# Kernel tuning notes

Measured on AMD Instinct MI355X. Metric: run time of the kernel, lower is better.

Reference implementation:

```python
import jax, jax.numpy as jnp
import numpy as np

THRESHOLD = 0.5
ALPHA = 1.0
N, D = 100000, 256
B, K = 1024, 128


def _l2norm(x):
    # F.normalize(x, p=2, dim=-1) with eps=1e-12
    return x / jnp.maximum(jnp.linalg.norm(x, axis=-1, keepdims=True), 1e-12)


def setup_inputs() -> dict:
    key = jax.random.key(0)
    k1, k2, k3, k4, k5, k6, k7 = jax.random.split(key, 7)
    feature = jax.random.normal(k1, (N, D), dtype=jnp.float32)
    text_embedding = jax.random.normal(k2, (N, D), dtype=jnp.float32)
    virtual = jax.random.normal(k3, (1, D), dtype=jnp.float32)
    # Gumbel(0,1) noise for gumbel_softmax (tau=1), materialized for determinism
    u = jax.random.uniform(k4, (B, K, K), dtype=jnp.float32, minval=1e-6, maxval=1.0 - 1e-6)
    gumbel = -jnp.log(-jnp.log(u))
    ego_nodes = jnp.sort(jax.random.randint(k5, (B, K), 0, N, dtype=jnp.int32), axis=-1)
    edges_adj = jax.random.randint(k6, (B, K, K), 0, 2, dtype=jnp.int32)
    train_label = jax.random.randint(k7, (B,), 0, 2, dtype=jnp.int32)
    return {"feature": feature, "text_embedding": text_embedding, "virtual": virtual,
            "gumbel": gumbel, "ego_nodes": ego_nodes, "edges_adj": edges_adj,
            "train_label": train_label}


def reference(feature, text_embedding, virtual, gumbel, ego_nodes, edges_adj, train_label):
    feat = _l2norm(feature)          # self.feature (normalized in __init__)
    emb = _l2norm(text_embedding)    # self.embedding
    te_local = _l2norm(emb - virtual)            # [N, D]

    tb = te_local[ego_nodes]                     # [B, K, D] gather per ego-subgraph
    sim = jnp.einsum('bkd,bjd->bkj', tb, tb) - THRESHOLD   # [B, K, K]
    sim_sub = jax.nn.softmax(sim + gumbel, axis=-1)         # gumbel_softmax, tau=1

    adj = edges_adj.astype(sim_sub.dtype)        # scatter edges_adj[src,dst]=1, precomputed
    # s_diff: row-wise L2 norm then mean over rows
    s_diff = jnp.sqrt(jnp.sum((adj - sim_sub) ** 2, axis=-1)).mean(axis=-1)   # [B]

    emb_out = feat[ego_nodes].mean(axis=1)       # [B, D] sum(feature)/n
    emb_pg = emb[ego_nodes].mean(axis=1)         # [B, D] sum(embedding)/n  (n == K)
    f_diff = jnp.linalg.norm(emb_out - emb_pg, axis=-1)                        # [B]

    score = s_diff + ALPHA * f_diff
    score = (score - score.min()) / (score.max() - score.min())

    y = train_label.astype(score.dtype)
    eps = 1e-7  # stabilizes log at exact 0/1 (torch BCELoss clamps log at -100)
    sc = jnp.clip(score, eps, 1.0 - eps)
    bce = -(y * jnp.log(sc) + (1.0 - y) * jnp.log1p(-sc)).mean()
    loss = bce / y.shape[0]
    return score, loss
```

## Files before the change

kernel.cpp:

```cpp
#include <hip/hip_runtime.h>
#include <hip/hip_bf16.h>
#include <math.h>

#define DIM 256
#define BB 1024
#define KK 128
#define PITCH 264

typedef __attribute__((ext_vector_type(8))) short short8;
typedef __attribute__((ext_vector_type(4))) float float4v;

__device__ __forceinline__ float dot4(const float4 a, const float4 b) {
    return a.x*b.x + a.y*b.y + a.z*b.z + a.w*b.w;
}

__device__ __forceinline__ unsigned bf2bits(float a, float b) {
    float2 t; t.x = a; t.y = b;
    __hip_bfloat162 h = __float22bfloat162_rn(t);
    unsigned u; __builtin_memcpy(&u, &h, 4);
    return u;
}

template<int CTRL>
__device__ __forceinline__ float addror(float x) {
    int r = __builtin_amdgcn_update_dpp(0, __float_as_int(x), CTRL, 0xF, 0xF, true);
    return x + __int_as_float(r);
}
__device__ __forceinline__ float sum16dpp(float x) {
    x = addror<0x121>(x);
    x = addror<0x122>(x);
    x = addror<0x124>(x);
    x = addror<0x128>(x);
    return x;
}
__device__ __forceinline__ float sum64dpp(float x) {
    x = sum16dpp(x);
    x += __shfl_xor(x, 16);
    x += __shfl_xor(x, 32);
    return x;
}

__global__ __launch_bounds__(512, 4) void fused_main(
    const float* __restrict__ feature,
    const float* __restrict__ text,
    const float* __restrict__ virt,
    const float* __restrict__ gumbel,
    const int*   __restrict__ ego,
    const int*   __restrict__ adj,
    float*       __restrict__ score_raw)
{
    __shared__ unsigned short tbs[KK * PITCH];
    __shared__ float fpart[8][DIM];
    __shared__ float rowpart[KK][8];
    __shared__ float spart[2];

    const int b    = blockIdx.x;
    const int tid  = threadIdx.x;
    const int wave = tid >> 6;
    const int lane = tid & 63;

    const float4 vm = ((const float4*)virt)[lane];
    const float vv2 = sum64dpp(dot4(vm, vm));

    const int* ego_b = ego + b * KK;
    const int  base  = wave * 16;

    float4 fdv = make_float4(0.f, 0.f, 0.f, 0.f);

    #pragma unroll
    for (int bt = 0; bt < 4; ++bt) {
        const int r0 = base + bt * 4;
        const int e0i = ego_b[r0 + 0], e1i = ego_b[r0 + 1];
        const int e2i = ego_b[r0 + 2], e3i = ego_b[r0 + 3];
        const float4 T0 = ((const float4*)(text + (size_t)e0i * DIM))[lane];
        const float4 T1 = ((const float4*)(text + (size_t)e1i * DIM))[lane];
        const float4 T2 = ((const float4*)(text + (size_t)e2i * DIM))[lane];
        const float4 T3 = ((const float4*)(text + (size_t)e3i * DIM))[lane];
        const float4 F0 = ((const float4*)(feature + (size_t)e0i * DIM))[lane];
        const float4 F1 = ((const float4*)(feature + (size_t)e1i * DIM))[lane];
        const float4 F2 = ((const float4*)(feature + (size_t)e2i * DIM))[lane];
        const float4 F3 = ((const float4*)(feature + (size_t)e3i * DIM))[lane];

        float st0 = dot4(T0, T0), sv0 = dot4(T0, vm), sf0 = dot4(F0, F0);
        float st1 = dot4(T1, T1), sv1 = dot4(T1, vm), sf1 = dot4(F1, F1);
        float st2 = dot4(T2, T2), sv2 = dot4(T2, vm), sf2 = dot4(F2, F2);
        float st3 = dot4(T3, T3), sv3 = dot4(T3, vm), sf3 = dot4(F3, F3);

        st0 = sum64dpp(st0); sv0 = sum64dpp(sv0); sf0 = sum64dpp(sf0);
        st1 = sum64dpp(st1); sv1 = sum64dpp(sv1); sf1 = sum64dpp(sf1);
        st2 = sum64dpp(st2); sv2 = sum64dpp(sv2); sf2 = sum64dpp(sf2);
        st3 = sum64dpp(st3); sv3 = sum64dpp(sv3); sf3 = sum64dpp(sf3);

        #define NORMROW(Tj, Fj, stj, sfj, svj, ROW)                              \
        {                                                                        \
            const float inv_ne = __builtin_amdgcn_rsqf(fmaxf(stj, 1e-24f));      \
            const float inv_nf = __builtin_amdgcn_rsqf(fmaxf(sfj, 1e-24f));      \
            const float nw2    = fmaxf(1.f + vv2 - 2.f * svj * inv_ne, 1e-24f);  \
            const float inv_nt = __builtin_amdgcn_rsqf(nw2);                     \
            const float e0 = Tj.x * inv_ne, e1 = Tj.y * inv_ne;                  \
            const float e2 = Tj.z * inv_ne, e3 = Tj.w * inv_ne;                  \
            fdv.x += Fj.x * inv_nf - e0;  fdv.y += Fj.y * inv_nf - e1;           \
            fdv.z += Fj.z * inv_nf - e2;  fdv.w += Fj.w * inv_nf - e3;           \
            uint2 pk;                                                            \
            pk.x = bf2bits((e0 - vm.x) * inv_nt, (e1 - vm.y) * inv_nt);          \
            pk.y = bf2bits((e2 - vm.z) * inv_nt, (e3 - vm.w) * inv_nt);          \
            *(uint2*)&tbs[(ROW) * PITCH + 4 * lane] = pk;                        \
        }
        NORMROW(T0, F0, st0, sf0, sv0, r0 + 0)
        NORMROW(T1, F1, st1, sf1, sv1, r0 + 1)
        NORMROW(T2, F2, st2, sf2, sv2, r0 + 2)
        NORMROW(T3, F3, st3, sf3, sv3, r0 + 3)
        #undef NORMROW
    }
    *(float4*)&fpart[wave][4 * lane] = fdv;

    __syncthreads();

    const int g = lane >> 4;
    const int c = lane & 15;

    #pragma unroll
    for (int h = 0; h < 2; ++h) {
        float4v acc[4];
        #pragma unroll
        for (int t = 0; t < 4; ++t) acc[t] = (float4v){0.f, 0.f, 0.f, 0.f};

        #pragma unroll
        for (int q = 0; q < 8; ++q) {
            const int dq = q * 32 + g * 8;
            const short8 afr = *(const short8*)&tbs[(base + c) * PITCH + dq];
            #pragma unroll
            for (int t = 0; t < 4; ++t) {
                const short8 bfr = *(const short8*)&tbs[(h * 64 + t * 16 + c) * PITCH + dq];
                acc[t] = __builtin_amdgcn_mfma_f32_16x16x32_bf16(afr, bfr, acc[t], 0, 0, 0);
            }
        }

        const float* gr = gumbel + ((size_t)b * KK + base + g * 4) * KK + h * 64 + c;
        const int*   ar = adj    + ((size_t)b * KK + base + g * 4) * KK + h * 64 + c;

        #pragma unroll
        for (int r = 0; r < 4; ++r) {
            int av0 = __builtin_nontemporal_load(ar + r * KK);
            int av1 = __builtin_nontemporal_load(ar + r * KK + 16);
            int av2 = __builtin_nontemporal_load(ar + r * KK + 32);
            int av3 = __builtin_nontemporal_load(ar + r * KK + 48);
            float gv0 = __builtin_nontemporal_load(gr + r * KK);
            float gv1 = __builtin_nontemporal_load(gr + r * KK + 16);
            float gv2 = __builtin_nontemporal_load(gr + r * KK + 32);
            float gv3 = __builtin_nontemporal_load(gr + r * KK + 48);

            const float et0 = __expf(acc[0][r] - 0.5f + gv0);
            const float et1 = __expf(acc[1][r] - 0.5f + gv1);
            const float et2 = __expf(acc[2][r] - 0.5f + gv2);
            const float et3 = __expf(acc[3][r] - 0.5f + gv3);

            float s   = et0 + et1 + et2 + et3;
            float a3  = et0*et0 + et1*et1 + et2*et2 + et3*et3;
            float a2  = (av0 ? et0 : 0.f) + (av1 ? et1 : 0.f)
                      + (av2 ? et2 : 0.f) + (av3 ? et3 : 0.f);
            float fia = (av0 ? 1.f : 0.f) + (av1 ? 1.f : 0.f)
                      + (av2 ? 1.f : 0.f) + (av3 ? 1.f : 0.f);

            s   = sum16dpp(s);
            a2  = sum16dpp(a2);
            a3  = sum16dpp(a3);
            fia = sum16dpp(fia);

            if (c == 0) {
                float4 pk4; pk4.x = s; pk4.y = a2; pk4.z = a3; pk4.w = fia;
                *(float4*)&rowpart[base + g * 4 + r][h * 4] = pk4;
            }
        }
    }

    __syncthreads();

    if (tid < KK) {
        const float4 pa = *(const float4*)&rowpart[tid][0];
        const float4 pb = *(const float4*)&rowpart[tid][4];
        const float s   = pa.x + pb.x;
        const float a2  = pa.y + pb.y;
        const float a3  = pa.z + pb.z;
        const float fia = pa.w + pb.w;
        const float invS = __builtin_amdgcn_rcpf(s);
        float sq = sqrtf(fmaxf(fia - invS * (2.f * a2 - invS * a3), 0.f));
        sq = sum64dpp(sq);
        if (lane == 0) spart[wave] = sq;
    }

    __syncthreads();

    if (wave == 0) {
        float4 d = make_float4(0.f, 0.f, 0.f, 0.f);
        #pragma unroll
        for (int j = 0; j < 8; ++j) {
            const float4 p = *(const float4*)&fpart[j][4 * lane];
            d.x += p.x; d.y += p.y; d.z += p.z; d.w += p.w;
        }
        const float inv = 1.f / 128.f;
        d.x *= inv; d.y *= inv; d.z *= inv; d.w *= inv;
        const float q2 = sum64dpp(dot4(d, d));
        if (lane == 0)
            score_raw[b] = (spart[0] + spart[1]) * (1.f / 128.f) + sqrtf(q2);
    }
}

__global__ __launch_bounds__(1024) void finalize(
    const float* __restrict__ score_raw,
    const int*   __restrict__ label,
    float*       __restrict__ out)
{
    __shared__ float wmin[16], wmax[16], wsum[16];
    const int tid = threadIdx.x;
    const float s = score_raw[tid];
    float mn = s, mx = s;
    #pragma unroll
    for (int m = 1; m < 64; m <<= 1) {
        mn = fminf(mn, __shfl_xor(mn, m));
        mx = fmaxf(mx, __shfl_xor(mx, m));
    }
    if ((tid & 63) == 0) { wmin[tid >> 6] = mn; wmax[tid >> 6] = mx; }
    __syncthreads();
    float gmn = wmin[0], gmx = wmax[0];
    #pragma unroll
    for (int w = 1; w < 16; ++w) {
        gmn = fminf(gmn, wmin[w]);
        gmx = fmaxf(gmx, wmax[w]);
    }
    const float score = (s - gmn) / (gmx - gmn);
    out[tid] = score;

    const float y  = (float)label[tid];
    const float sc = fminf(fmaxf(score, 1e-7f), 1.f - 1e-7f);
    float term = -(y * logf(sc) + (1.f - y) * log1pf(-sc));
    #pragma unroll
    for (int m = 1; m < 64; m <<= 1) term += __shfl_xor(term, m);
    if ((tid & 63) == 0) wsum[tid >> 6] = term;
    __syncthreads();
    if (tid == 0) {
        float tot = 0.f;
        #pragma unroll
        for (int w = 0; w < 16; ++w) tot += wsum[w];
        out[BB] = tot / (1024.f * 1024.f);
    }
}

extern "C" void kernel_launch(void* const* d_in, const int* in_sizes, int n_in,
                              void* d_out, int out_size, void* d_ws, size_t ws_size,
                              hipStream_t stream) {
    const float* feature = (const float*)d_in[0];
    const float* text    = (const float*)d_in[1];
    const float* virt    = (const float*)d_in[2];
    const float* gumbel  = (const float*)d_in[3];
    const int*   ego     = (const int*)d_in[4];
    const int*   adj     = (const int*)d_in[5];
    const int*   label   = (const int*)d_in[6];
    float* out       = (float*)d_out;
    float* score_raw = (float*)d_ws;

    fused_main<<<BB, 512, 0, stream>>>(feature, text, virt, gumbel, ego, adj, score_raw);
    finalize<<<1, 1024, 0, stream>>>(score_raw, label, out);
}
```

Baseline: 70.11 us.

## Prefetch adjacency as packed bits during gather phase and hoist gumbel loads

The adjacency matrix is now loaded with 16-byte vector loads during the embedding gather/normalize phase and packed into a per-row bitmask in shared memory. The softmax epilogue reads these bits and counts set entries with popcount instead of issuing scalar int loads and a DPP reduction. Gumbel loads for each half are issued before the MFMA loop so their latency overlaps the matrix multiply. The feature-difference partials are also pre-reduced pairwise into half as many shared-memory slots. The cost is extra registers for the prefetched gumbel values and one more shared array.

```diff
diff --git a/kernel.cpp b/kernel.cpp
--- a/kernel.cpp
+++ b/kernel.cpp
@@ -9,6 +9,7 @@
 
 typedef __attribute__((ext_vector_type(8))) short short8;
 typedef __attribute__((ext_vector_type(4))) float float4v;
+typedef __attribute__((ext_vector_type(4))) int int4v;
 
 __device__ __forceinline__ float dot4(const float4 a, const float4 b) {
     return a.x*b.x + a.y*b.y + a.z*b.z + a.w*b.w;
@@ -50,8 +51,9 @@
     float*       __restrict__ score_raw)
 {
     __shared__ unsigned short tbs[KK * PITCH];
-    __shared__ float fpart[8][DIM];
+    __shared__ float fpart[4][DIM];
     __shared__ float rowpart[KK][8];
+    __shared__ unsigned abits[KK][4];
     __shared__ float spart[2];
 
     const int b    = blockIdx.x;
@@ -64,6 +66,9 @@
 
     const int* ego_b = ego + b * KK;
     const int  base  = wave * 16;
+
+    const int* apk = adj + (size_t)b * KK * KK + (tid >> 2) * KK + (tid & 3) * 32;
+    unsigned abreg = 0;
 
     float4 fdv = make_float4(0.f, 0.f, 0.f, 0.f);
 
@@ -80,6 +85,8 @@
         const float4 F1 = ((const float4*)(feature + (size_t)e1i * DIM))[lane];
         const float4 F2 = ((const float4*)(feature + (size_t)e2i * DIM))[lane];
         const float4 F3 = ((const float4*)(feature + (size_t)e3i * DIM))[lane];
+        const int4v A0 = __builtin_nontemporal_load((const int4v*)(apk + bt * 8));
+        const int4v A1 = __builtin_nontemporal_load((const int4v*)(apk + bt * 8 + 4));
 
         float st0 = dot4(T0, T0), sv0 = dot4(T0, vm), sf0 = dot4(F0, F0);
         float st1 = dot4(T1, T1), sv1 = dot4(T1, vm), sf1 = dot4(F1, F1);
@@ -111,16 +118,42 @@
         NORMROW(T2, F2, st2, sf2, sv2, r0 + 2)
         NORMROW(T3, F3, st3, sf3, sv3, r0 + 3)
         #undef NORMROW
-    }
-    *(float4*)&fpart[wave][4 * lane] = fdv;
-
-    __syncthreads();
+
+        abreg |= (A0.x ? 1u : 0u) << (bt * 8 + 0);
+        abreg |= (A0.y ? 1u : 0u) << (bt * 8 + 1);
+        abreg |= (A0.z ? 1u : 0u) << (bt * 8 + 2);
+        abreg |= (A0.w ? 1u : 0u) << (bt * 8 + 3);
+        abreg |= (A1.x ? 1u : 0u) << (bt * 8 + 4);
+        abreg |= (A1.y ? 1u : 0u) << (bt * 8 + 5);
+        abreg |= (A1.z ? 1u : 0u) << (bt * 8 + 6);
+        abreg |= (A1.w ? 1u : 0u) << (bt * 8 + 7);
+    }
+    abits[tid >> 2][tid & 3] = abreg;
+    if (wave & 1) *(float4*)&fpart[wave >> 1][4 * lane] = fdv;
+
+    __syncthreads();
+
+    if (!(wave & 1)) {
+        float4 o = *(float4*)&fpart[wave >> 1][4 * lane];
+        o.x += fdv.x; o.y += fdv.y; o.z += fdv.z; o.w += fdv.w;
+        *(float4*)&fpart[wave >> 1][4 * lane] = o;
+    }
 
     const int g = lane >> 4;
     const int c = lane & 15;
+    const float* grb = gumbel + ((size_t)b * KK + base + g * 4) * KK + c;
 
     #pragma unroll
     for (int h = 0; h < 2; ++h) {
+        float gvv[16];
+        #pragma unroll
+        for (int r = 0; r < 4; ++r) {
+            #pragma unroll
+            for (int t = 0; t < 4; ++t)
+                gvv[r * 4 + t] =
+                    __builtin_nontemporal_load(grb + r * KK + h * 64 + t * 16);
+        }
+
         float4v acc[4];
         #pragma unroll
         for (int t = 0; t < 4; ++t) acc[t] = (float4v){0.f, 0.f, 0.f, 0.f};
@@ -136,36 +169,24 @@
             }
         }
 
-        const float* gr = gumbel + ((size_t)b * KK + base + g * 4) * KK + h * 64 + c;
-        const int*   ar = adj    + ((size_t)b * KK + base + g * 4) * KK + h * 64 + c;
-
         #pragma unroll
         for (int r = 0; r < 4; ++r) {
-            int av0 = __builtin_nontemporal_load(ar + r * KK);
-            int av1 = __builtin_nontemporal_load(ar + r * KK + 16);
-            int av2 = __builtin_nontemporal_load(ar + r * KK + 32);
-            int av3 = __builtin_nontemporal_load(ar + r * KK + 48);
-            float gv0 = __builtin_nontemporal_load(gr + r * KK);
-            float gv1 = __builtin_nontemporal_load(gr + r * KK + 16);
-            float gv2 = __builtin_nontemporal_load(gr + r * KK + 32);
-            float gv3 = __builtin_nontemporal_load(gr + r * KK + 48);
-
-            const float et0 = __expf(acc[0][r] - 0.5f + gv0);
-            const float et1 = __expf(acc[1][r] - 0.5f + gv1);
-            const float et2 = __expf(acc[2][r] - 0.5f + gv2);
-            const float et3 = __expf(acc[3][r] - 0.5f + gv3);
-
-            float s   = et0 + et1 + et2 + et3;
-            float a3  = et0*et0 + et1*et1 + et2*et2 + et3*et3;
-            float a2  = (av0 ? et0 : 0.f) + (av1 ? et1 : 0.f)
-                      + (av2 ? et2 : 0.f) + (av3 ? et3 : 0.f);
-            float fia = (av0 ? 1.f : 0.f) + (av1 ? 1.f : 0.f)
-                      + (av2 ? 1.f : 0.f) + (av3 ? 1.f : 0.f);
-
-            s   = sum16dpp(s);
-            a2  = sum16dpp(a2);
-            a3  = sum16dpp(a3);
-            fia = sum16dpp(fia);
+            const uint2 aw = *(const uint2*)&abits[base + g * 4 + r][h * 2];
+
+            float s = 0.f, a2 = 0.f, a3 = 0.f;
+            #pragma unroll
+            for (int t = 0; t < 4; ++t) {
+                const float et = __expf(acc[t][r] - 0.5f + gvv[r * 4 + t]);
+                const unsigned w  = (t < 2) ? aw.x : aw.y;
+                const unsigned bit = (w >> ((t & 1) * 16 + c)) & 1u;
+                s  += et;
+                a3 += et * et;
+                a2 += bit ? et : 0.f;
+            }
+            s  = sum16dpp(s);
+            a2 = sum16dpp(a2);
+            a3 = sum16dpp(a3);
+            const float fia = (float)(__popc(aw.x) + __popc(aw.y));
 
             if (c == 0) {
                 float4 pk4; pk4.x = s; pk4.y = a2; pk4.z = a3; pk4.w = fia;
@@ -194,7 +215,7 @@
     if (wave == 0) {
         float4 d = make_float4(0.f, 0.f, 0.f, 0.f);
         #pragma unroll
-        for (int j = 0; j < 8; ++j) {
+        for (int j = 0; j < 4; ++j) {
             const float4 p = *(const float4*)&fpart[j][4 * lane];
             d.x += p.x; d.y += p.y; d.z += p.z; d.w += p.w;
         }
```

After: 86.01 us. 1.23x slower.
